# Kernel optimization log

Measured on AMD Instinct MI355X. Metric: run time of the kernel, lower is better.

The kernel has to match this reference:

```python
import jax, jax.numpy as jnp
import numpy as np

START = 1
NUM_CLASSES = 64  # labels drawn from [0, 64)
EPS = 1e-12       # matches F.normalize eps


def _compactness_loss(embeddings, labels):
    # L2-normalize each embedding (F.normalize, dim=-1)
    norms = jnp.maximum(jnp.linalg.norm(embeddings, axis=-1, keepdims=True), EPS)
    emb = embeddings / norms  # [N, D]

    ones = jnp.ones((emb.shape[0],), dtype=emb.dtype)
    counts = jax.ops.segment_sum(ones, labels, num_segments=NUM_CLASSES)      # [C]
    sums = jax.ops.segment_sum(emb, labels, num_segments=NUM_CLASSES)         # [C, D]

    # per-class mean, then L2-normalize the center (F.normalize, dim=1)
    centers = sums / jnp.maximum(counts, 1.0)[:, None]
    c_norms = jnp.maximum(jnp.linalg.norm(centers, axis=-1, keepdims=True), EPS)
    centers = centers / c_norms  # [C, D]

    # cosine similarity of each sample to its own class center
    sim = jnp.sum(emb * centers[labels], axis=-1)  # [N]

    # per-class mean of (1 - sim), only classes with count > 1 contribute
    per_class_sum = jax.ops.segment_sum(1.0 - sim, labels, num_segments=NUM_CLASSES)  # [C]
    valid = counts > 1.0
    class_loss = jnp.where(valid, per_class_sum / jnp.maximum(counts, 1.0), 0.0)
    n_valid = jnp.sum(valid.astype(emb.dtype))
    return jnp.where(n_valid > 0, jnp.sum(class_loss) / jnp.maximum(n_valid, 1.0), 0.0)


def setup_inputs() -> dict:
    key = jax.random.key(0)
    k1, k2 = jax.random.split(key)
    N, D = 262144, 256
    embeddings = jax.random.normal(k1, (N, D), dtype=jnp.float32)
    labels = jax.random.randint(k2, (N,), 0, NUM_CLASSES, dtype=jnp.int64)
    return {"embeddings": embeddings, "labels": labels, "epoch": 5}


def reference(embeddings, labels, epoch):
    if epoch < START:  # epoch is a static python int
        return jnp.asarray(0.0, dtype=embeddings.dtype)
    return _compactness_loss(embeddings, labels)
```

## Files before the change

### kernel.cpp

```cpp
#include <hip/hip_runtime.h>

#define CLS 64
#define DIM 256
#define NB  256
#define WIN 1024
#define MT  1024
#define WPB 16
#define CPW 4
#define P2  4

typedef float f32x4 __attribute__((ext_vector_type(4)));

__device__ __forceinline__ float wave_sum64(float f) {
    int t;
    t = __builtin_amdgcn_update_dpp(0, __float_as_int(f), 0x111, 0xf, 0xf, false); f += __int_as_float(t);
    t = __builtin_amdgcn_update_dpp(0, __float_as_int(f), 0x112, 0xf, 0xf, false); f += __int_as_float(t);
    t = __builtin_amdgcn_update_dpp(0, __float_as_int(f), 0x114, 0xf, 0xe, false); f += __int_as_float(t);
    t = __builtin_amdgcn_update_dpp(0, __float_as_int(f), 0x118, 0xf, 0xc, false); f += __int_as_float(t);
    t = __builtin_amdgcn_update_dpp(0, __float_as_int(f), 0x142, 0xa, 0xf, false); f += __int_as_float(t);
    t = __builtin_amdgcn_update_dpp(0, __float_as_int(f), 0x143, 0xc, 0xf, false); f += __int_as_float(t);
    return __int_as_float(__builtin_amdgcn_readlane(__float_as_int(f), 63));
}

__global__ __launch_bounds__(MT) void k_main(
    const float* __restrict__ emb, const int* __restrict__ labels, int N,
    float* __restrict__ partials,
    float* __restrict__ cnts)
{
    __shared__ unsigned short lst[WPB][WIN];
    __shared__ int lcnt[WPB];

    const int tid  = threadIdx.x;
    const int w    = tid >> 6;
    const int lane = tid & 63;
    const int b    = blockIdx.x;

    f32x4 a0 = {0,0,0,0}, a1 = {0,0,0,0}, a2 = {0,0,0,0}, a3 = {0,0,0,0};
    float c0 = 0.f, c1 = 0.f, c2 = 0.f, c3 = 0.f;

    for (long long base = (long long)b * WIN; base < N; base += (long long)NB * WIN) {
        const int nrows = (int)min((long long)WIN, (long long)N - base);
        __syncthreads();
        if (tid < WPB) lcnt[tid] = 0;
        __syncthreads();
        if (tid < nrows) {
            const int lab = labels[base + tid];
            const int g = lab >> 2;
            const int pos = atomicAdd(&lcnt[g], 1);
            lst[g][pos] = (unsigned short)(tid | ((lab & 3) << 10));
        }
        __syncthreads();

        const int n = lcnt[w];
        const float* embb = emb + (size_t)base * DIM;
        int j = 0;
        for (; j + 4 <= n; j += 4) {
            const unsigned long long e4 =
                *reinterpret_cast<const unsigned long long*>(&lst[w][j]);
            const int e0 = __builtin_amdgcn_readfirstlane((int)( e4        & 0xffff));
            const int e1 = __builtin_amdgcn_readfirstlane((int)((e4 >> 16) & 0xffff));
            const int e2 = __builtin_amdgcn_readfirstlane((int)((e4 >> 32) & 0xffff));
            const int e3 = __builtin_amdgcn_readfirstlane((int)((e4 >> 48) & 0xffff));
            const f32x4 v0 = *(reinterpret_cast<const f32x4*>(embb + (size_t)(e0 & 1023) * DIM) + lane);
            const f32x4 v1 = *(reinterpret_cast<const f32x4*>(embb + (size_t)(e1 & 1023) * DIM) + lane);
            const f32x4 v2 = *(reinterpret_cast<const f32x4*>(embb + (size_t)(e2 & 1023) * DIM) + lane);
            const f32x4 v3 = *(reinterpret_cast<const f32x4*>(embb + (size_t)(e3 & 1023) * DIM) + lane);
            const float s0 = wave_sum64(v0.x*v0.x + v0.y*v0.y + v0.z*v0.z + v0.w*v0.w);
            const float s1 = wave_sum64(v1.x*v1.x + v1.y*v1.y + v1.z*v1.z + v1.w*v1.w);
            const float s2 = wave_sum64(v2.x*v2.x + v2.y*v2.y + v2.z*v2.z + v2.w*v2.w);
            const float s3 = wave_sum64(v3.x*v3.x + v3.y*v3.y + v3.z*v3.z + v3.w*v3.w);
            const float i0 = 1.0f / fmaxf(sqrtf(s0), 1e-12f);
            const float i1 = 1.0f / fmaxf(sqrtf(s1), 1e-12f);
            const float i2 = 1.0f / fmaxf(sqrtf(s2), 1e-12f);
            const float i3 = 1.0f / fmaxf(sqrtf(s3), 1e-12f);
            {   f32x4 t; t.x = v0.x*i0; t.y = v0.y*i0; t.z = v0.z*i0; t.w = v0.w*i0;
                const int k = e0 >> 10;
                if      (k == 0) { a0 += t; c0 += 1.f; }
                else if (k == 1) { a1 += t; c1 += 1.f; }
                else if (k == 2) { a2 += t; c2 += 1.f; }
                else             { a3 += t; c3 += 1.f; } }
            {   f32x4 t; t.x = v1.x*i1; t.y = v1.y*i1; t.z = v1.z*i1; t.w = v1.w*i1;
                const int k = e1 >> 10;
                if      (k == 0) { a0 += t; c0 += 1.f; }
                else if (k == 1) { a1 += t; c1 += 1.f; }
                else if (k == 2) { a2 += t; c2 += 1.f; }
                else             { a3 += t; c3 += 1.f; } }
            {   f32x4 t; t.x = v2.x*i2; t.y = v2.y*i2; t.z = v2.z*i2; t.w = v2.w*i2;
                const int k = e2 >> 10;
                if      (k == 0) { a0 += t; c0 += 1.f; }
                else if (k == 1) { a1 += t; c1 += 1.f; }
                else if (k == 2) { a2 += t; c2 += 1.f; }
                else             { a3 += t; c3 += 1.f; } }
            {   f32x4 t; t.x = v3.x*i3; t.y = v3.y*i3; t.z = v3.z*i3; t.w = v3.w*i3;
                const int k = e3 >> 10;
                if      (k == 0) { a0 += t; c0 += 1.f; }
                else if (k == 1) { a1 += t; c1 += 1.f; }
                else if (k == 2) { a2 += t; c2 += 1.f; }
                else             { a3 += t; c3 += 1.f; } }
        }
        for (; j < n; ++j) {
            const int e = __builtin_amdgcn_readfirstlane((int)lst[w][j]);
            const f32x4 v = *(reinterpret_cast<const f32x4*>(embb + (size_t)(e & 1023) * DIM) + lane);
            const float ss  = wave_sum64(v.x*v.x + v.y*v.y + v.z*v.z + v.w*v.w);
            const float inv = 1.0f / fmaxf(sqrtf(ss), 1e-12f);
            f32x4 t; t.x = v.x*inv; t.y = v.y*inv; t.z = v.z*inv; t.w = v.w*inv;
            const int k = e >> 10;
            if      (k == 0) { a0 += t; c0 += 1.f; }
            else if (k == 1) { a1 += t; c1 += 1.f; }
            else if (k == 2) { a2 += t; c2 += 1.f; }
            else             { a3 += t; c3 += 1.f; }
        }
    }

    *reinterpret_cast<f32x4*>(partials + ((size_t)(w*CPW + 0) * NB + b) * DIM + 4*lane) = a0;
    *reinterpret_cast<f32x4*>(partials + ((size_t)(w*CPW + 1) * NB + b) * DIM + 4*lane) = a1;
    *reinterpret_cast<f32x4*>(partials + ((size_t)(w*CPW + 2) * NB + b) * DIM + 4*lane) = a2;
    *reinterpret_cast<f32x4*>(partials + ((size_t)(w*CPW + 3) * NB + b) * DIM + 4*lane) = a3;
    if (lane == 0) {
        cnts[(size_t)(w*CPW + 0) * NB + b] = c0;
        cnts[(size_t)(w*CPW + 1) * NB + b] = c1;
        cnts[(size_t)(w*CPW + 2) * NB + b] = c2;
        cnts[(size_t)(w*CPW + 3) * NB + b] = c3;
    }
}

__global__ __launch_bounds__(256) void k_reduce1(
    const float* __restrict__ partials, float* __restrict__ red1)
{
    const int c = blockIdx.x >> 2;
    const int p = blockIdx.x & (P2 - 1);
    const int d = threadIdx.x;
    const float* src = partials + ((size_t)c * NB + p * (NB / P2)) * DIM + d;
    float s = 0.f;
    #pragma unroll 8
    for (int bb = 0; bb < NB / P2; ++bb) s += src[(size_t)bb * DIM];
    red1[((size_t)c * P2 + p) * DIM + d] = s;
}

__global__ __launch_bounds__(256) void k_classloss(
    const float* __restrict__ red1, const float* __restrict__ cnts,
    float* __restrict__ closs, float* __restrict__ cvalid)
{
    const int c = blockIdx.x;
    const int d = threadIdx.x;
    float s = 0.f;
    #pragma unroll
    for (int p = 0; p < P2; ++p) s += red1[((size_t)c * P2 + p) * DIM + d];
    const float w2 = wave_sum64(s * s);
    const float cw = wave_sum64(cnts[(size_t)c * NB + d]);
    __shared__ float reds[4], redc[4];
    if ((d & 63) == 0) { reds[d >> 6] = w2; redc[d >> 6] = cw; }
    __syncthreads();
    if (d == 0) {
        float s2   = reds[0] + reds[1] + reds[2] + reds[3];
        float cnt  = redc[0] + redc[1] + redc[2] + redc[3];
        float invc = 1.0f / fmaxf(cnt, 1.0f);
        float cn   = sqrtf(s2) * invc;
        float dot  = s2 * invc / fmaxf(cn, 1e-12f);
        float pcs  = cnt - dot;
        bool valid = cnt > 1.0f;
        closs[c]  = valid ? pcs * invc : 0.0f;
        cvalid[c] = valid ? 1.0f : 0.0f;
    }
}

__global__ void k_final(const float* __restrict__ closs, const float* __restrict__ cvalid,
                        const int* __restrict__ epoch, float* __restrict__ out)
{
    const int t = threadIdx.x;
    const float sl = wave_sum64(closs[t]);
    const float nv = wave_sum64(cvalid[t]);
    if (t == 0) {
        float res = (nv > 0.0f) ? (sl / fmaxf(nv, 1.0f)) : 0.0f;
        if (epoch[0] < 1) res = 0.0f;
        out[0] = res;
    }
}

extern "C" void kernel_launch(void* const* d_in, const int* in_sizes, int n_in,
                              void* d_out, int out_size, void* d_ws, size_t ws_size,
                              hipStream_t stream)
{
    const float* emb    = (const float*)d_in[0];
    const int*   labels = (const int*)d_in[1];
    const int*   epoch  = (const int*)d_in[2];
    float*       out    = (float*)d_out;
    const int N = in_sizes[0] / DIM;

    char* ws = (char*)d_ws;
    size_t off = 0;
    auto carve = [&](size_t bytes) { size_t o = off; off = (off + bytes + 255) & ~(size_t)255; return o; };
    float* partials = (float*)(ws + carve((size_t)CLS * NB * DIM * sizeof(float)));
    float* cnts     = (float*)(ws + carve((size_t)CLS * NB * sizeof(float)));
    float* red1     = (float*)(ws + carve((size_t)CLS * P2 * DIM * sizeof(float)));
    float* closs    = (float*)(ws + carve((size_t)CLS * sizeof(float)));
    float* cvalid   = (float*)(ws + carve((size_t)CLS * sizeof(float)));
    (void)ws_size;

    k_main     <<<NB,       MT,  0, stream>>>(emb, labels, N, partials, cnts);
    k_reduce1  <<<CLS * P2, 256, 0, stream>>>(partials, red1);
    k_classloss<<<CLS,      256, 0, stream>>>(red1, cnts, closs, cvalid);
    k_final    <<<1,        64,  0, stream>>>(closs, cvalid, epoch, out);
}
```

Measured before the change: 62.70 us.

## Stage normalized rows in double-buffered LDS and scan labels with ballot

Measured after the change: 75.51 us. +20.4%, slower.

```diff
diff --git a/kernel.cpp b/kernel.cpp
--- a/kernel.cpp
+++ b/kernel.cpp
@@ -7,6 +7,7 @@
 #define MT  1024
 #define WPB 16
 #define CPW 4
+#define SC  64
 #define P2  4
 
 typedef float f32x4 __attribute__((ext_vector_type(4)));
@@ -27,8 +28,7 @@
     float* __restrict__ partials,
     float* __restrict__ cnts)
 {
-    __shared__ unsigned short lst[WPB][WIN];
-    __shared__ int lcnt[WPB];
+    __shared__ float buf[2][SC][DIM];
 
     const int tid  = threadIdx.x;
     const int w    = tid >> 6;
@@ -38,77 +38,72 @@
     f32x4 a0 = {0,0,0,0}, a1 = {0,0,0,0}, a2 = {0,0,0,0}, a3 = {0,0,0,0};
     float c0 = 0.f, c1 = 0.f, c2 = 0.f, c3 = 0.f;
 
-    for (long long base = (long long)b * WIN; base < N; base += (long long)NB * WIN) {
-        const int nrows = (int)min((long long)WIN, (long long)N - base);
-        __syncthreads();
-        if (tid < WPB) lcnt[tid] = 0;
-        __syncthreads();
-        if (tid < nrows) {
-            const int lab = labels[base + tid];
-            const int g = lab >> 2;
-            const int pos = atomicAdd(&lcnt[g], 1);
-            lst[g][pos] = (unsigned short)(tid | ((lab & 3) << 10));
+    for (long long wbase = (long long)b * WIN; wbase < N; wbase += (long long)NB * WIN) {
+        const int wrows = (int)min((long long)WIN, (long long)N - wbase);
+        const int nsc   = (wrows + SC - 1) / SC;
+
+        {
+            const long long rb = wbase + 4 * w;
+            #pragma unroll
+            for (int i = 0; i < 4; ++i) {
+                f32x4 v = {0,0,0,0};
+                if (rb + i < N)
+                    v = *(reinterpret_cast<const f32x4*>(emb + (size_t)(rb + i) * DIM) + lane);
+                const float ss  = wave_sum64(v.x*v.x + v.y*v.y + v.z*v.z + v.w*v.w);
+                const float inv = 1.0f / fmaxf(sqrtf(ss), 1e-12f);
+                f32x4 t; t.x = v.x*inv; t.y = v.y*inv; t.z = v.z*inv; t.w = v.w*inv;
+                *reinterpret_cast<f32x4*>(&buf[0][4*w + i][4*lane]) = t;
+            }
         }
         __syncthreads();
 
-        const int n = lcnt[w];
-        const float* embb = emb + (size_t)base * DIM;
-        int j = 0;
-        for (; j + 4 <= n; j += 4) {
-            const unsigned long long e4 =
-                *reinterpret_cast<const unsigned long long*>(&lst[w][j]);
-            const int e0 = __builtin_amdgcn_readfirstlane((int)( e4        & 0xffff));
-            const int e1 = __builtin_amdgcn_readfirstlane((int)((e4 >> 16) & 0xffff));
-            const int e2 = __builtin_amdgcn_readfirstlane((int)((e4 >> 32) & 0xffff));
-            const int e3 = __builtin_amdgcn_readfirstlane((int)((e4 >> 48) & 0xffff));
-            const f32x4 v0 = *(reinterpret_cast<const f32x4*>(embb + (size_t)(e0 & 1023) * DIM) + lane);
-            const f32x4 v1 = *(reinterpret_cast<const f32x4*>(embb + (size_t)(e1 & 1023) * DIM) + lane);
-            const f32x4 v2 = *(reinterpret_cast<const f32x4*>(embb + (size_t)(e2 & 1023) * DIM) + lane);
-            const f32x4 v3 = *(reinterpret_cast<const f32x4*>(embb + (size_t)(e3 & 1023) * DIM) + lane);
-            const float s0 = wave_sum64(v0.x*v0.x + v0.y*v0.y + v0.z*v0.z + v0.w*v0.w);
-            const float s1 = wave_sum64(v1.x*v1.x + v1.y*v1.y + v1.z*v1.z + v1.w*v1.w);
-            const float s2 = wave_sum64(v2.x*v2.x + v2.y*v2.y + v2.z*v2.z + v2.w*v2.w);
-            const float s3 = wave_sum64(v3.x*v3.x + v3.y*v3.y + v3.z*v3.z + v3.w*v3.w);
-            const float i0 = 1.0f / fmaxf(sqrtf(s0), 1e-12f);
-            const float i1 = 1.0f / fmaxf(sqrtf(s1), 1e-12f);
-            const float i2 = 1.0f / fmaxf(sqrtf(s2), 1e-12f);
-            const float i3 = 1.0f / fmaxf(sqrtf(s3), 1e-12f);
-            {   f32x4 t; t.x = v0.x*i0; t.y = v0.y*i0; t.z = v0.z*i0; t.w = v0.w*i0;
-                const int k = e0 >> 10;
-                if      (k == 0) { a0 += t; c0 += 1.f; }
-                else if (k == 1) { a1 += t; c1 += 1.f; }
-                else if (k == 2) { a2 += t; c2 += 1.f; }
-                else             { a3 += t; c3 += 1.f; } }
-            {   f32x4 t; t.x = v1.x*i1; t.y = v1.y*i1; t.z = v1.z*i1; t.w = v1.w*i1;
-                const int k = e1 >> 10;
-                if      (k == 0) { a0 += t; c0 += 1.f; }
-                else if (k == 1) { a1 += t; c1 += 1.f; }
-                else if (k == 2) { a2 += t; c2 += 1.f; }
-                else             { a3 += t; c3 += 1.f; } }
-            {   f32x4 t; t.x = v2.x*i2; t.y = v2.y*i2; t.z = v2.z*i2; t.w = v2.w*i2;
-                const int k = e2 >> 10;
-                if      (k == 0) { a0 += t; c0 += 1.f; }
-                else if (k == 1) { a1 += t; c1 += 1.f; }
-                else if (k == 2) { a2 += t; c2 += 1.f; }
-                else             { a3 += t; c3 += 1.f; } }
-            {   f32x4 t; t.x = v3.x*i3; t.y = v3.y*i3; t.z = v3.z*i3; t.w = v3.w*i3;
-                const int k = e3 >> 10;
-                if      (k == 0) { a0 += t; c0 += 1.f; }
-                else if (k == 1) { a1 += t; c1 += 1.f; }
-                else if (k == 2) { a2 += t; c2 += 1.f; }
-                else             { a3 += t; c3 += 1.f; } }
-        }
-        for (; j < n; ++j) {
-            const int e = __builtin_amdgcn_readfirstlane((int)lst[w][j]);
-            const f32x4 v = *(reinterpret_cast<const f32x4*>(embb + (size_t)(e & 1023) * DIM) + lane);
-            const float ss  = wave_sum64(v.x*v.x + v.y*v.y + v.z*v.z + v.w*v.w);
-            const float inv = 1.0f / fmaxf(sqrtf(ss), 1e-12f);
-            f32x4 t; t.x = v.x*inv; t.y = v.y*inv; t.z = v.z*inv; t.w = v.w*inv;
-            const int k = e >> 10;
-            if      (k == 0) { a0 += t; c0 += 1.f; }
-            else if (k == 1) { a1 += t; c1 += 1.f; }
-            else if (k == 2) { a2 += t; c2 += 1.f; }
-            else             { a3 += t; c3 += 1.f; }
+        for (int s = 0; s < nsc; ++s) {
+            const int  cur = s & 1;
+            const bool hn  = (s + 1 < nsc);
+
+            f32x4 r0 = {0,0,0,0}, r1 = {0,0,0,0}, r2 = {0,0,0,0}, r3 = {0,0,0,0};
+            const long long rb = wbase + (long long)(s + 1) * SC + 4 * w;
+            if (hn) {
+                if (rb + 0 < N) r0 = *(reinterpret_cast<const f32x4*>(emb + (size_t)(rb + 0) * DIM) + lane);
+                if (rb + 1 < N) r1 = *(reinterpret_cast<const f32x4*>(emb + (size_t)(rb + 1) * DIM) + lane);
+                if (rb + 2 < N) r2 = *(reinterpret_cast<const f32x4*>(emb + (size_t)(rb + 2) * DIM) + lane);
+                if (rb + 3 < N) r3 = *(reinterpret_cast<const f32x4*>(emb + (size_t)(rb + 3) * DIM) + lane);
+            }
+
+            const long long cb = wbase + (long long)s * SC;
+            const int lab = (cb + lane < N) ? labels[cb + lane] : -1;
+            unsigned long long mask = __ballot((lab >> 2) == w);
+            while (mask) {
+                const int r = (int)__builtin_ctzll(mask);
+                mask &= mask - 1;
+                const int k = __builtin_amdgcn_readlane(lab, r) & 3;
+                const f32x4 v = *reinterpret_cast<const f32x4*>(&buf[cur][r][4*lane]);
+                if      (k == 0) { a0 += v; c0 += 1.f; }
+                else if (k == 1) { a1 += v; c1 += 1.f; }
+                else if (k == 2) { a2 += v; c2 += 1.f; }
+                else             { a3 += v; c3 += 1.f; }
+            }
+
+            if (hn) {
+                const float s0 = wave_sum64(r0.x*r0.x + r0.y*r0.y + r0.z*r0.z + r0.w*r0.w);
+                const float s1 = wave_sum64(r1.x*r1.x + r1.y*r1.y + r1.z*r1.z + r1.w*r1.w);
+                const float s2 = wave_sum64(r2.x*r2.x + r2.y*r2.y + r2.z*r2.z + r2.w*r2.w);
+                const float s3 = wave_sum64(r3.x*r3.x + r3.y*r3.y + r3.z*r3.z + r3.w*r3.w);
+                const float i0 = 1.0f / fmaxf(sqrtf(s0), 1e-12f);
+                const float i1 = 1.0f / fmaxf(sqrtf(s1), 1e-12f);
+                const float i2 = 1.0f / fmaxf(sqrtf(s2), 1e-12f);
+                const float i3 = 1.0f / fmaxf(sqrtf(s3), 1e-12f);
+                f32x4 t;
+                t.x = r0.x*i0; t.y = r0.y*i0; t.z = r0.z*i0; t.w = r0.w*i0;
+                *reinterpret_cast<f32x4*>(&buf[cur ^ 1][4*w + 0][4*lane]) = t;
+                t.x = r1.x*i1; t.y = r1.y*i1; t.z = r1.z*i1; t.w = r1.w*i1;
+                *reinterpret_cast<f32x4*>(&buf[cur ^ 1][4*w + 1][4*lane]) = t;
+                t.x = r2.x*i2; t.y = r2.y*i2; t.z = r2.z*i2; t.w = r2.w*i2;
+                *reinterpret_cast<f32x4*>(&buf[cur ^ 1][4*w + 2][4*lane]) = t;
+                t.x = r3.x*i3; t.y = r3.y*i3; t.z = r3.z*i3; t.w = r3.w*i3;
+                *reinterpret_cast<f32x4*>(&buf[cur ^ 1][4*w + 3][4*lane]) = t;
+            }
+            __syncthreads();
         }
     }
 
```
